# Performance work log

Hardware: AMD Instinct MI355X
Metric: run time of the kernel (lower is better)

Reference implementation:

```python
import jax, jax.numpy as jnp
import numpy as np
import math

D_MODEL = 1024
N_HEAD = 16
D_FF = 4096
B, T, S = 2, 2048, 2048
LN_EPS = 1e-5


def _linear(x, w, b):
    # torch nn.Linear: y = x @ W.T + b, W: [out, in]
    return jnp.einsum('bsd,od->bso', x, w) + b


def _layer_norm(x, g, b):
    mu = jnp.mean(x, axis=-1, keepdims=True)
    var = jnp.var(x, axis=-1, keepdims=True)
    return (x - mu) * jax.lax.rsqrt(var + LN_EPS) * g + b


def _mha(xq, xkv, wq, bq, wk, bk, wv, bv, wo, bo, mask):
    Bq, Tq, D = xq.shape
    Tk = xkv.shape[1]
    dk = D // N_HEAD
    q = _linear(xq, wq, bq).reshape(Bq, Tq, N_HEAD, dk).transpose(0, 2, 1, 3)
    k = _linear(xkv, wk, bk).reshape(Bq, Tk, N_HEAD, dk).transpose(0, 2, 1, 3)
    v = _linear(xkv, wv, bv).reshape(Bq, Tk, N_HEAD, dk).transpose(0, 2, 1, 3)
    scores = jnp.einsum('bhqd,bhkd->bhqk', q, k) / math.sqrt(dk)
    if mask is not None:
        scores = jnp.where(mask == 0, jnp.asarray(-1e9, scores.dtype), scores)
    attn = jax.nn.softmax(scores, axis=-1)  # dropout is eval-mode identity
    out = jnp.einsum('bhqk,bhkd->bhqd', attn, v)
    out = out.transpose(0, 2, 1, 3).reshape(Bq, Tq, D)
    return _linear(out, wo, bo)


def setup_inputs() -> dict:
    key = jax.random.key(0)
    ks = jax.random.split(key, 20)
    sd = 0.02

    def w(k, shape):
        return (jax.random.normal(k, shape, dtype=jnp.float32) * sd)

    inp = {
        'x': jax.random.normal(ks[0], (B, T, D_MODEL), dtype=jnp.float32),
        'enc_output': jax.random.normal(ks[1], (B, S, D_MODEL), dtype=jnp.float32),
        # causal (future) mask for self-attention
        'tgt_mask': jnp.tril(jnp.ones((T, T), dtype=jnp.int32))[None, None, :, :].repeat(B, axis=0),
        # no source padding -> all ones
        'src_tgt_mask': jnp.ones((B, 1, T, S), dtype=jnp.int32),
        'sa_wq': w(ks[2], (D_MODEL, D_MODEL)), 'sa_bq': jnp.zeros((D_MODEL,), jnp.float32),
        'sa_wk': w(ks[3], (D_MODEL, D_MODEL)), 'sa_bk': jnp.zeros((D_MODEL,), jnp.float32),
        'sa_wv': w(ks[4], (D_MODEL, D_MODEL)), 'sa_bv': jnp.zeros((D_MODEL,), jnp.float32),
        'sa_wo': w(ks[5], (D_MODEL, D_MODEL)), 'sa_bo': jnp.zeros((D_MODEL,), jnp.float32),
        'ca_wq': w(ks[6], (D_MODEL, D_MODEL)), 'ca_bq': jnp.zeros((D_MODEL,), jnp.float32),
        'ca_wk': w(ks[7], (D_MODEL, D_MODEL)), 'ca_bk': jnp.zeros((D_MODEL,), jnp.float32),
        'ca_wv': w(ks[8], (D_MODEL, D_MODEL)), 'ca_bv': jnp.zeros((D_MODEL,), jnp.float32),
        'ca_wo': w(ks[9], (D_MODEL, D_MODEL)), 'ca_bo': jnp.zeros((D_MODEL,), jnp.float32),
        'ffn_w1': w(ks[10], (D_FF, D_MODEL)), 'ffn_b1': jnp.zeros((D_FF,), jnp.float32),
        'ffn_w2': w(ks[11], (D_MODEL, D_FF)), 'ffn_b2': jnp.zeros((D_MODEL,), jnp.float32),
        'ln1_g': jnp.ones((D_MODEL,), jnp.float32), 'ln1_b': jnp.zeros((D_MODEL,), jnp.float32),
        'ln2_g': jnp.ones((D_MODEL,), jnp.float32), 'ln2_b': jnp.zeros((D_MODEL,), jnp.float32),
        'ln3_g': jnp.ones((D_MODEL,), jnp.float32), 'ln3_b': jnp.zeros((D_MODEL,), jnp.float32),
    }
    return inp


def reference(x, enc_output, tgt_mask, src_tgt_mask,
              sa_wq, sa_bq, sa_wk, sa_bk, sa_wv, sa_bv, sa_wo, sa_bo,
              ca_wq, ca_bq, ca_wk, ca_bk, ca_wv, ca_bv, ca_wo, ca_bo,
              ffn_w1, ffn_b1, ffn_w2, ffn_b2,
              ln1_g, ln1_b, ln2_g, ln2_b, ln3_g, ln3_b):
    # masked self-attention + residual + LN
    a1 = _mha(x, x, sa_wq, sa_bq, sa_wk, sa_bk, sa_wv, sa_bv, sa_wo, sa_bo, tgt_mask)
    x = _layer_norm(x + a1, ln1_g, ln1_b)
    # cross-attention + residual + LN
    a2 = _mha(x, enc_output, ca_wq, ca_bq, ca_wk, ca_bk, ca_wv, ca_bv, ca_wo, ca_bo, src_tgt_mask)
    x = _layer_norm(x + a2, ln2_g, ln2_b)
    # FFN + residual + LN
    h = jax.nn.relu(_linear(x, ffn_w1, ffn_b1))
    f = _linear(h, ffn_w2, ffn_b2)
    x = _layer_norm(x + f, ln3_g, ln3_b)
    return x
```

## Files before the change

### kernel.cpp

```cpp
#include <hip/hip_runtime.h>
#include <stdint.h>

typedef uint16_t u16;
typedef __attribute__((ext_vector_type(8))) short short8;
typedef __attribute__((ext_vector_type(4))) short short4v;
typedef __attribute__((ext_vector_type(4))) float f32x4;
typedef __attribute__((ext_vector_type(2))) unsigned int u32x2;

#define GLB_AS __attribute__((address_space(1)))
#define LDS_AS __attribute__((address_space(3)))

__device__ __forceinline__ void gload_lds16(const void* g, void* l) {
  __builtin_amdgcn_global_load_lds((GLB_AS void*)(g), (LDS_AS void*)(l), 16, 0, 0);
}

__device__ __forceinline__ float bf2f(u16 u) {
  union { uint32_t i; float f; } v; v.i = ((uint32_t)u) << 16; return v.f;
}
__device__ __forceinline__ u16 f2bf(float f) {
  uint32_t x = __builtin_bit_cast(uint32_t, f);
  return (u16)((x + 0x7fffu + ((x >> 16) & 1u)) >> 16);
}
__device__ __forceinline__ uint32_t cvtpk(float lo, float hi) {
  uint32_t r;
  asm("v_cvt_pk_bf16_f32 %0, %1, %2" : "=v"(r) : "v"(lo), "v"(hi));
  return r;
}

struct CastJobs {
  const float* s[12];
  u16* d[12];
  int n[12];
};
__global__ __launch_bounds__(256) void cast_many(CastJobs j)
{
  const int job = blockIdx.y;
  const int i = (blockIdx.x * 256 + threadIdx.x) * 4;
  if (i >= j.n[job]) return;
  const float4 v = *(const float4*)(j.s[job] + i);
  short4v r;
  r[0] = (short)f2bf(v.x); r[1] = (short)f2bf(v.y);
  r[2] = (short)f2bf(v.z); r[3] = (short)f2bf(v.w);
  *(short4v*)(j.d[job] + i) = r;
}

__global__ __launch_bounds__(256) void vtrans(
    const u16* __restrict__ V, int vs, u16* __restrict__ Vt)
{
  __shared__ u16 tl[64][72];
  const int tid = threadIdx.x;
  const int b = blockIdx.z, h = blockIdx.y, t0 = blockIdx.x * 64;
#pragma unroll
  for (int it = 0; it < 2; ++it) {
    const int r = (tid >> 3) + it*32, c = (tid & 7) * 8;
    short8 vv = *(const short8*)(V + (size_t)(b*2048 + t0 + r)*vs + h*64 + c);
    *(short8*)(&tl[r][c]) = vv;
  }
  __syncthreads();
#pragma unroll
  for (int it = 0; it < 2; ++it) {
    const int d = (tid >> 3) + it*32, t8 = (tid & 7) * 8;
    short8 ov;
#pragma unroll
    for (int j = 0; j < 8; ++j) ov[j] = (short)tl[t8 + j][d];
    *(short8*)(Vt + ((size_t)((b*16 + h)*64 + d))*2048 + t0 + t8) = ov;
  }
}

template<int RELU, int NSEG, int BN, int SCALEQ>
__global__ __launch_bounds__(256) void gemm_bt(
    const u16* __restrict__ A, const u16* __restrict__ W,
    const float* __restrict__ b0, const float* __restrict__ b1,
    const float* __restrict__ b2, u16* __restrict__ Y,
    int M, int N, int K)
{
  constexpr int NBUF = (BN == 64) ? 3 : 2;
  __shared__ __attribute__((aligned(16))) u16 lA[NBUF][128*64];
  __shared__ __attribute__((aligned(16))) u16 lB[NBUF][BN*64];
  const int tid  = threadIdx.x;
  const int lane = tid & 63, wv = tid >> 6;
  constexpr int WM = (BN == 128) ? 64 : 32;
  constexpr int MI = WM / 16;
  constexpr int BRND = BN / 32;
  const int wm = (BN == 128) ? (wv >> 1) : wv;
  const int wn = (BN == 128) ? (wv & 1) : 0;
  const int l16 = lane & 15, l4 = lane >> 4;
  const int rswz = (l16 & 7) << 4;

  const int gx = gridDim.x;
  int flat = blockIdx.y * gx + blockIdx.x;
  flat = (flat & 7) * ((gx * gridDim.y) >> 3) + (flat >> 3);
  const int bx = (flat % gx) * BN, by = (flat / gx) * 128;

  const f32x4 fzero = {0.f, 0.f, 0.f, 0.f};
  f32x4 acc[MI][4];
#pragma unroll
  for (int i = 0; i < MI; ++i)
#pragma unroll
    for (int j = 0; j < 4; ++j) acc[i][j] = fzero;

  const int o = wv*1024 + lane*16;

  auto stage = [&](int k0, int buf) {
#pragma unroll
    for (int r = 0; r < 4; ++r) {
      const int oo = r*4096 + o;
      const int row = oo >> 7;
      const int src = ((oo & 127) ^ ((row & 7) << 4)) >> 1;
      gload_lds16(A + (size_t)(by + row)*K + (k0 + src), (char*)lA[buf] + oo);
    }
#pragma unroll
    for (int r = 0; r < BRND; ++r) {
      const int oo = r*4096 + o;
      const int row = oo >> 7;
      const int src = ((oo & 127) ^ ((row & 7) << 4)) >> 1;
      gload_lds16(W + (size_t)(bx + row)*K + (k0 + src), (char*)lB[buf] + oo);
    }
  };

  auto compute = [&](int cur) {
    short8 af[2][MI], bfv[2][4];
#pragma unroll
    for (int ks = 0; ks < 2; ++ks) {
      const int cb = (ks*64 + l4*16) ^ rswz;
#pragma unroll
      for (int i = 0; i < MI; ++i)
        af[ks][i]  = *(const short8*)((const char*)lA[cur] + (wm*WM + i*16 + l16)*128 + cb);
#pragma unroll
      for (int j = 0; j < 4; ++j)
        bfv[ks][j] = *(const short8*)((const char*)lB[cur] + (wn*64 + j*16 + l16)*128 + cb);
    }
#pragma unroll
    for (int ks = 0; ks < 2; ++ks)
#pragma unroll
      for (int i = 0; i < MI; ++i)
#pragma unroll
        for (int j = 0; j < 4; ++j)
          acc[i][j] = __builtin_amdgcn_mfma_f32_16x16x32_bf16(af[ks][i], bfv[ks][j], acc[i][j], 0, 0, 0);
  };

  const int KT = K >> 6;
  if constexpr (BN == 64) {
    stage(0, 0);
    int cur = 0;
    for (int kt = 0; kt < KT; ++kt) {
      const int nxt = (cur + 1 == 3) ? 0 : cur + 1;
      if (kt + 1 < KT) {
        stage((kt + 1) << 6, nxt);
        asm volatile("s_waitcnt vmcnt(6)" ::: "memory");
      } else {
        asm volatile("s_waitcnt vmcnt(0)" ::: "memory");
      }
      __builtin_amdgcn_s_barrier();
      __builtin_amdgcn_sched_barrier(0);
      compute(cur);
      cur = nxt;
    }
  } else {
    stage(0, 0);
    for (int kt = 0; kt < KT; ++kt) {
      const int cur = kt & 1;
      __syncthreads();
      short8 af[2][MI], bfv[2][4];
#pragma unroll
      for (int ks = 0; ks < 2; ++ks) {
        const int cb = (ks*64 + l4*16) ^ rswz;
#pragma unroll
        for (int i = 0; i < MI; ++i)
          af[ks][i]  = *(const short8*)((const char*)lA[cur] + (wm*WM + i*16 + l16)*128 + cb);
#pragma unroll
        for (int j = 0; j < 4; ++j)
          bfv[ks][j] = *(const short8*)((const char*)lB[cur] + (wn*64 + j*16 + l16)*128 + cb);
      }
      if (kt + 1 < KT) stage((kt + 1) << 6, cur ^ 1);
#pragma unroll
      for (int ks = 0; ks < 2; ++ks)
#pragma unroll
        for (int i = 0; i < MI; ++i)
#pragma unroll
          for (int j = 0; j < 4; ++j)
            acc[i][j] = __builtin_amdgcn_mfma_f32_16x16x32_bf16(af[ks][i], bfv[ks][j], acc[i][j], 0, 0, 0);
    }
  }

  const float SCLF = 0.18033688f;
#pragma unroll
  for (int j = 0; j < 4; ++j) {
    const int col = bx + wn*64 + j*16 + l16;
    float bv;
    int seg = 0;
    if (NSEG == 1) bv = b0[col];
    else {
      seg = col >> 10;
      const int off = col & 1023;
      const float* bp = (seg == 0) ? b0 : ((seg == 1) ? b1 : b2);
      bv = bp[off];
    }
#pragma unroll
    for (int i = 0; i < MI; ++i) {
      const int r0 = by + wm*WM + i*16 + l4*4;
#pragma unroll
      for (int r = 0; r < 4; ++r) {
        float v = acc[i][j][r] + bv;
        if (RELU) v = v > 0.f ? v : 0.f;
        if (SCALEQ && (NSEG == 1 || seg == 0)) v *= SCLF;
        Y[(size_t)(r0 + r)*N + col] = f2bf(v);
      }
    }
  }
}

template<int CAUSAL, int QR>
__global__ __launch_bounds__(512, (QR == 16) ? 4 : 2) void attn_fwd(
    const u16* __restrict__ Q, int qs,
    const u16* __restrict__ K, int ks_,
    const u16* __restrict__ Vt, u16* __restrict__ O, int Tk)
{
  constexpr int NG = QR / 16;
  __shared__ __attribute__((aligned(16))) u16 lK[2][128*64];
  __shared__ __attribute__((aligned(16))) u16 lV[2][64*128];
  __shared__ __attribute__((aligned(16))) u16 lP[8][NG*1024];
  const int tid  = threadIdx.x;
  const int lane = tid & 63, wv = tid >> 6;
  const int l16 = lane & 15, l4 = lane >> 4;
  const int b = blockIdx.z, h = blockIdx.y;
  int strip;
  if (CAUSAL) {
    const int u = (blockIdx.x + blockIdx.z) & 15;
    strip = (u & 1) ? (15 - (u >> 1)) : (u >> 1);
  } else {
    strip = blockIdx.x;
  }
  const int Bq = strip * (8 * QR);
  const int qrow = Bq + wv*QR;

  short8 qf[NG][2];
#pragma unroll
  for (int g = 0; g < NG; ++g) {
    const u16* Qb = Q + (size_t)(b*2048 + qrow + g*16 + l16)*qs + h*64;
#pragma unroll
    for (int ks = 0; ks < 2; ++ks)
      qf[g][ks] = *(const short8*)(Qb + ks*32 + l4*8);
  }

  const f32x4 fzero = {0.f, 0.f, 0.f, 0.f};
  f32x4 accO[NG][4];
#pragma unroll
  for (int g = 0; g < NG; ++g)
#pragma unroll
    for (int i = 0; i < 4; ++i) accO[g][i] = fzero;
  float lrow[NG];
#pragma unroll
  for (int g = 0; g < NG; ++g) lrow[g] = 0.f;

  const int kend = CAUSAL ? (Bq + 8*QR) : Tk;
  const int nt = kend >> 7;
  const int qmax = qrow + QR - 1;
  const int srK = tid >> 3;
  const int scK = 8 * ((tid & 7) ^ (srK & 7));
  const int srV = tid >> 4;
  const int scV = 8 * ((tid & 15) ^ (srV & 7));
  const u16* KbG = K  + (size_t)(b*2048)*ks_ + h*64 + scK;
  const u16* VbG = Vt + ((size_t)((b*16 + h)*64 + srV))*2048 + scV;
  const int wvoff = (tid >> 6) * 1024;
  const int rswz = (l16 & 7) << 4;
  const int sbq = (lane & 48) + l4*4;

  char* const pbuf = (char*)lP + (tid >> 6) * (NG*2048);
  const int swzP = (l16 & 7) << 4;
  int wrA[4], rdA[2];
#pragma unroll
  for (int nf = 0; nf < 4; ++nf) wrA[nf] = l16*128 + ((nf*32 + l4*8) ^ swzP);
#pragma unroll
  for (int c = 0; c < 2; ++c)    rdA[c] = l16*128 + ((c*64 + l4*16) ^ swzP);

  auto readK = [&](int h2, int bb, short8 (&kf)[4][2]) {
#pragma unroll
    for (int nf = 0; nf < 4; ++nf) {
      const char* base = (const char*)lK[bb] + (h2*64 + nf*16 + l16)*128;
      kf[nf][0] = *(const short8*)(base + ((l4*16)      ^ rswz));
      kf[nf][1] = *(const short8*)(base + ((64 + l4*16) ^ rswz));
    }
  };

  auto compute64 = [&](int h2, int kvb, short8 (&kf)[4][2], int bb) {
#pragma unroll
    for (int g = 0; g < NG; ++g) {
      f32x4 sf[4];
      __builtin_amdgcn_s_setprio(1);
#pragma unroll
      for (int nf = 0; nf < 4; ++nf) {
        f32x4 s = fzero;
        s = __builtin_amdgcn_mfma_f32_16x16x32_bf16(kf[nf][0], qf[g][0], s, 0, 0, 0);
        s = __builtin_amdgcn_mfma_f32_16x16x32_bf16(kf[nf][1], qf[g][1], s, 0, 0, 0);
        sf[nf] = s;
      }
      __builtin_amdgcn_s_setprio(0);
      if (CAUSAL && (kvb + 63 > qrow + g*16)) {
        const int q = qrow + g*16 + l16;
#pragma unroll
        for (int nf = 0; nf < 4; ++nf)
#pragma unroll
          for (int r = 0; r < 4; ++r) {
            const int kv = kvb + nf*16 + l4*4 + r;
            if (kv > q) sf[nf][r] = -1e30f;
          }
      }
#pragma unroll
      for (int nf = 0; nf < 4; ++nf)
#pragma unroll
        for (int r = 0; r < 4; ++r)
          sf[nf][r] = exp2f(sf[nf][r]);
      float sm[4];
#pragma unroll
      for (int nf = 0; nf < 4; ++nf)
        sm[nf] = (sf[nf][0] + sf[nf][1]) + (sf[nf][2] + sf[nf][3]);
      lrow[g] += (sm[0] + sm[1]) + (sm[2] + sm[3]);
#pragma unroll
      for (int nf = 0; nf < 4; ++nf) {
        u32x2 w;
        w[0] = cvtpk(sf[nf][0], sf[nf][1]);
        w[1] = cvtpk(sf[nf][2], sf[nf][3]);
        *(u32x2*)(pbuf + g*2048 + wrA[nf]) = w;
      }
    }
#pragma unroll
    for (int c = 0; c < 2; ++c) {
      short8 pa[NG];
#pragma unroll
      for (int g = 0; g < NG; ++g)
        pa[g] = *(const short8*)(pbuf + g*2048 + rdA[c]);
      __builtin_amdgcn_s_setprio(1);
#pragma unroll
      for (int df = 0; df < 4; ++df) {
        const short8 vf = *(const short8*)((const char*)lV[bb] +
            (df*16 + l16)*256 + ((h2*128 + c*64 + l4*16) ^ rswz));
#pragma unroll
        for (int g = 0; g < NG; ++g)
          accO[g][df] = __builtin_amdgcn_mfma_f32_16x16x32_bf16(pa[g], vf, accO[g][df], 0, 0, 0);
      }
      __builtin_amdgcn_s_setprio(0);
    }
  };

#pragma unroll
  for (int r = 0; r < 2; ++r) {
    gload_lds16(KbG + (size_t)(r*64 + srK)*ks_, (char*)lK[0] + r*8192 + wvoff);
    gload_lds16(VbG + (size_t)(r*32)*2048,      (char*)lV[0] + r*8192 + wvoff);
  }

  for (int t = 0; t < nt; ++t) {
    const int bb = t & 1;
    const int kb = t << 7;
    __syncthreads();
    short8 kf[4][2];
    readK(0, bb, kf);
    if (t + 1 < nt) {
      const int kb2 = kb + 128;
#pragma unroll
      for (int r = 0; r < 2; ++r) {
        gload_lds16(KbG + (size_t)(kb2 + r*64 + srK)*ks_,
                    (char*)lK[bb^1] + r*8192 + wvoff);
        gload_lds16(VbG + (size_t)(r*32)*2048 + kb2,
                    (char*)lV[bb^1] + r*8192 + wvoff);
      }
    }
    compute64(0, kb, kf, bb);
    if (!CAUSAL || (kb + 64 <= qmax)) {
      readK(1, bb, kf);
      compute64(1, kb + 64, kf, bb);
    }
  }

#pragma unroll
  for (int g = 0; g < NG; ++g) {
    lrow[g] += __shfl_xor(lrow[g], 16);
    lrow[g] += __shfl_xor(lrow[g], 32);
    u16* Ob = O + (size_t)(b*2048 + qrow + g*16 + l4*4)*1024 + h*64;
#pragma unroll
    for (int r = 0; r < 4; ++r) {
      const float inv = 1.f / __shfl(lrow[g], sbq + r);
#pragma unroll
      for (int df = 0; df < 4; ++df)
        Ob[(size_t)r*1024 + df*16 + l16] = f2bf(accO[g][df][r] * inv);
    }
  }
}

template<int XF32, int OF32>
__global__ __launch_bounds__(256) void add_ln(
    const void* __restrict__ Xp, const u16* __restrict__ R,
    const float* __restrict__ G, const float* __restrict__ Bb,
    void* __restrict__ OUTp)
{
  const int row = blockIdx.x;
  const int tid = threadIdx.x;
  const size_t base = (size_t)row*1024 + tid*4;
  float xv[4];
  if (XF32) {
    const float4 t = *(const float4*)((const float*)Xp + base);
    xv[0] = t.x; xv[1] = t.y; xv[2] = t.z; xv[3] = t.w;
  } else {
    short4v t = *(const short4v*)((const u16*)Xp + base);
#pragma unroll
    for (int i = 0; i < 4; ++i) xv[i] = bf2f((u16)t[i]);
  }
  short4v rv = *(const short4v*)(R + base);
  float v[4], s = 0.f, s2 = 0.f;
#pragma unroll
  for (int i = 0; i < 4; ++i) {
    float t = xv[i] + bf2f((u16)rv[i]);
    v[i] = t; s += t; s2 += t*t;
  }
#pragma unroll
  for (int m = 1; m < 64; m <<= 1) { s += __shfl_xor(s, m); s2 += __shfl_xor(s2, m); }
  __shared__ float red[8];
  const int w = tid >> 6, lane = tid & 63;
  if (lane == 0) { red[w] = s; red[4 + w] = s2; }
  __syncthreads();
  s  = red[0] + red[1] + red[2] + red[3];
  s2 = red[4] + red[5] + red[6] + red[7];
  const float mu  = s * (1.f/1024.f);
  const float var = s2 * (1.f/1024.f) - mu*mu;
  const float rs  = rsqrtf(var + 1e-5f);
  if (OF32) {
    float4 ov;
    ov.x = (v[0]-mu)*rs*G[tid*4+0] + Bb[tid*4+0];
    ov.y = (v[1]-mu)*rs*G[tid*4+1] + Bb[tid*4+1];
    ov.z = (v[2]-mu)*rs*G[tid*4+2] + Bb[tid*4+2];
    ov.w = (v[3]-mu)*rs*G[tid*4+3] + Bb[tid*4+3];
    *(float4*)((float*)OUTp + base) = ov;
  } else {
    short4v ov;
#pragma unroll
    for (int i = 0; i < 4; ++i)
      ov[i] = (short)f2bf((v[i] - mu)*rs*G[tid*4+i] + Bb[tid*4+i]);
    *(short4v*)((u16*)OUTp + base) = ov;
  }
}

extern "C" void kernel_launch(void* const* d_in, const int* in_sizes, int n_in,
                              void* d_out, int out_size, void* d_ws, size_t ws_size,
                              hipStream_t stream)
{
  (void)in_sizes; (void)n_in; (void)out_size;
  const float* x    = (const float*)d_in[0];
  const float* enc  = (const float*)d_in[1];
  const float* sa_wq = (const float*)d_in[4];  const float* sa_bq = (const float*)d_in[5];
  const float* sa_wk = (const float*)d_in[6];  const float* sa_bk = (const float*)d_in[7];
  const float* sa_wv = (const float*)d_in[8];  const float* sa_bv = (const float*)d_in[9];
  const float* sa_wo = (const float*)d_in[10]; const float* sa_bo = (const float*)d_in[11];
  const float* ca_wq = (const float*)d_in[12]; const float* ca_bq = (const float*)d_in[13];
  const float* ca_wk = (const float*)d_in[14]; const float* ca_bk = (const float*)d_in[15];
  const float* ca_wv = (const float*)d_in[16]; const float* ca_bv = (const float*)d_in[17];
  const float* ca_wo = (const float*)d_in[18]; const float* ca_bo = (const float*)d_in[19];
  const float* w1 = (const float*)d_in[20];    const float* b1 = (const float*)d_in[21];
  const float* w2 = (const float*)d_in[22];    const float* b2 = (const float*)d_in[23];
  const float* ln1g = (const float*)d_in[24];  const float* ln1b = (const float*)d_in[25];
  const float* ln2g = (const float*)d_in[26];  const float* ln2b = (const float*)d_in[27];
  const float* ln3g = (const float*)d_in[28];  const float* ln3b = (const float*)d_in[29];
  float* out = (float*)d_out;

  char* ws = (char*)d_ws;
  const size_t MB = 1024*1024;
  u16* xb   = (u16*)(ws);
  u16* encb = (u16*)(ws + 8*MB);
  u16* wsab = (u16*)(ws + 16*MB);
  u16* wcab = (u16*)(ws + 24*MB);
  u16* x1   = (u16*)(ws + 32*MB);
  u16* ao   = (u16*)(ws + 40*MB);
  u16* tmp  = (u16*)(ws + 48*MB);
  u16* vt   = (u16*)(ws + 56*MB);
  u16* qkv  = (u16*)(ws + 64*MB);
  u16* kvb  = (u16*)(ws + 88*MB);
  u16* x2   = xb;
  u16* hb   = qkv;

  const bool bigws = ws_size >= (size_t)120*MB;
  u16* w1b = bigws ? (u16*)(ws + 104*MB) : encb;
  u16* w2b = bigws ? (u16*)(ws + 112*MB) : vt;

  const int NW = 1024*1024;
  const int NX = 4096*1024;
  dim3 blk(256);

  {
    CastJobs cj{};
    cj.s[0] = x;     cj.d[0] = xb;           cj.n[0] = NX;
    cj.s[1] = enc;   cj.d[1] = encb;         cj.n[1] = NX;
    cj.s[2] = sa_wq; cj.d[2] = wsab + 0*NW;  cj.n[2] = NW;
    cj.s[3] = sa_wk; cj.d[3] = wsab + 1*NW;  cj.n[3] = NW;
    cj.s[4] = sa_wv; cj.d[4] = wsab + 2*NW;  cj.n[4] = NW;
    cj.s[5] = sa_wo; cj.d[5] = wsab + 3*NW;  cj.n[5] = NW;
    cj.s[6] = ca_wq; cj.d[6] = wcab + 0*NW;  cj.n[6] = NW;
    cj.s[7] = ca_wk; cj.d[7] = wcab + 1*NW;  cj.n[7] = NW;
    cj.s[8] = ca_wv; cj.d[8] = wcab + 2*NW;  cj.n[8] = NW;
    cj.s[9] = ca_wo; cj.d[9] = wcab + 3*NW;  cj.n[9] = NW;
    int njobs = 10;
    if (bigws) {
      cj.s[10] = w1; cj.d[10] = w1b; cj.n[10] = NX;
      cj.s[11] = w2; cj.d[11] = w2b; cj.n[11] = NX;
      njobs = 12;
    }
    cast_many<<<dim3(NX/1024, njobs), blk, 0, stream>>>(cj);
  }

  const int M = 4096;
  dim3 gN64(16, 32);
  dim3 gQKV(24, 32);
  dim3 gKV(16, 32);
  dim3 gF1(32, 32);
  dim3 gAttn(16, 16, 2);
  dim3 gT(32, 16, 2);
  dim3 blk512(512);

  gemm_bt<0,3,128,1><<<gQKV, blk, 0, stream>>>(xb, wsab, sa_bq, sa_bk, sa_bv, qkv, M, 3072, 1024);
  vtrans<<<gT, blk, 0, stream>>>(qkv + 2048, 3072, vt);
  attn_fwd<1,16><<<gAttn, blk512, 0, stream>>>(qkv, 3072, qkv + 1024, 3072, vt, ao, 2048);
  gemm_bt<0,1,64,0><<<gN64, blk, 0, stream>>>(ao, wsab + 3*NW, sa_bo, sa_bo, sa_bo, tmp, M, 1024, 1024);
  add_ln<1,0><<<4096, blk, 0, stream>>>(x, tmp, ln1g, ln1b, x1);

  gemm_bt<0,1,64,1><<<gN64, blk, 0, stream>>>(x1, wcab + 0*NW, ca_bq, ca_bq, ca_bq, qkv, M, 1024, 1024);
  gemm_bt<0,2,128,0><<<gKV, blk, 0, stream>>>(encb, wcab + 1*NW, ca_bk, ca_bv, ca_bv, kvb, M, 2048, 1024);
  vtrans<<<gT, blk, 0, stream>>>(kvb + 1024, 2048, vt);
  attn_fwd<0,16><<<gAttn, blk512, 0, stream>>>(qkv, 1024, kvb, 2048, vt, ao, 2048);
  if (!bigws) {
    CastJobs cj{};
    cj.s[0] = w1; cj.d[0] = w1b; cj.n[0] = NX;
    cj.s[1] = w2; cj.d[1] = w2b; cj.n[1] = NX;
    cast_many<<<dim3(NX/1024, 2), blk, 0, stream>>>(cj);
  }
  gemm_bt<0,1,64,0><<<gN64, blk, 0, stream>>>(ao, wcab + 3*NW, ca_bo, ca_bo, ca_bo, tmp, M, 1024, 1024);
  add_ln<0,0><<<4096, blk, 0, stream>>>(x1, tmp, ln2g, ln2b, x2);

  gemm_bt<1,1,128,0><<<gF1, blk, 0, stream>>>(x2, w1b, b1, b1, b1, hb, M, 4096, 1024);
  gemm_bt<0,1,64,0><<<gN64, blk, 0, stream>>>(hb, w2b, b2, b2, b2, tmp, M, 1024, 4096);
  add_ln<0,1><<<4096, blk, 0, stream>>>(x2, tmp, ln3g, ln3b, out);
}
```

Before: 327.7 us.

## Load K/V fragments directly from global in attention, drop LDS staging

Rewrites the attention kernel to use 256-thread blocks that each cover 64 query rows. K and V^T MFMA fragments now come straight from global memory into registers, with K prefetched one 64-key tile ahead, instead of being double-buffered through LDS with async global-to-LDS loads and block barriers. This removes the __syncthreads and LDS traffic for K/V and doubles the number of blocks in the grid. In exchange each wave re-reads K/V from global/L2 independently, losing sharing across waves, and the loads are strided rows rather than coalesced tiles.

```diff
diff --git a/kernel.cpp b/kernel.cpp
--- a/kernel.cpp
+++ b/kernel.cpp
@@ -210,63 +210,54 @@
   }
 }
 
-template<int CAUSAL, int QR>
-__global__ __launch_bounds__(512, (QR == 16) ? 4 : 2) void attn_fwd(
+template<int CAUSAL>
+__global__ __launch_bounds__(256) void attn_fwd(
     const u16* __restrict__ Q, int qs,
     const u16* __restrict__ K, int ks_,
     const u16* __restrict__ Vt, u16* __restrict__ O, int Tk)
 {
-  constexpr int NG = QR / 16;
-  __shared__ __attribute__((aligned(16))) u16 lK[2][128*64];
-  __shared__ __attribute__((aligned(16))) u16 lV[2][64*128];
-  __shared__ __attribute__((aligned(16))) u16 lP[8][NG*1024];
+  __shared__ __attribute__((aligned(16))) u16 lP[4][1024];
   const int tid  = threadIdx.x;
   const int lane = tid & 63, wv = tid >> 6;
   const int l16 = lane & 15, l4 = lane >> 4;
   const int b = blockIdx.z, h = blockIdx.y;
   int strip;
   if (CAUSAL) {
-    const int u = (blockIdx.x + blockIdx.z) & 15;
-    strip = (u & 1) ? (15 - (u >> 1)) : (u >> 1);
+    const int u = (blockIdx.x + blockIdx.z) & 31;
+    strip = (u & 1) ? (31 - (u >> 1)) : (u >> 1);
   } else {
     strip = blockIdx.x;
   }
-  const int Bq = strip * (8 * QR);
-  const int qrow = Bq + wv*QR;
-
-  short8 qf[NG][2];
-#pragma unroll
-  for (int g = 0; g < NG; ++g) {
-    const u16* Qb = Q + (size_t)(b*2048 + qrow + g*16 + l16)*qs + h*64;
-#pragma unroll
-    for (int ks = 0; ks < 2; ++ks)
-      qf[g][ks] = *(const short8*)(Qb + ks*32 + l4*8);
-  }
+  const int Bq = strip * 64;
+  const int qrow = Bq + wv*16;
+
+  const u16* Qb = Q + (size_t)(b*2048 + qrow + l16)*qs + h*64;
+  short8 qf[2];
+#pragma unroll
+  for (int ks = 0; ks < 2; ++ks)
+    qf[ks] = *(const short8*)(Qb + ks*32 + l4*8);
 
   const f32x4 fzero = {0.f, 0.f, 0.f, 0.f};
-  f32x4 accO[NG][4];
-#pragma unroll
-  for (int g = 0; g < NG; ++g)
-#pragma unroll
-    for (int i = 0; i < 4; ++i) accO[g][i] = fzero;
-  float lrow[NG];
-#pragma unroll
-  for (int g = 0; g < NG; ++g) lrow[g] = 0.f;
-
-  const int kend = CAUSAL ? (Bq + 8*QR) : Tk;
-  const int nt = kend >> 7;
-  const int qmax = qrow + QR - 1;
-  const int srK = tid >> 3;
-  const int scK = 8 * ((tid & 7) ^ (srK & 7));
-  const int srV = tid >> 4;
-  const int scV = 8 * ((tid & 15) ^ (srV & 7));
-  const u16* KbG = K  + (size_t)(b*2048)*ks_ + h*64 + scK;
-  const u16* VbG = Vt + ((size_t)((b*16 + h)*64 + srV))*2048 + scV;
-  const int wvoff = (tid >> 6) * 1024;
-  const int rswz = (l16 & 7) << 4;
+  f32x4 accO[4];
+#pragma unroll
+  for (int i = 0; i < 4; ++i) accO[i] = fzero;
+  float lrow = 0.f;
+
+  const int kend = CAUSAL ? (Bq + 64) : Tk;
+  const int nt = kend >> 6;
   const int sbq = (lane & 48) + l4*4;
 
-  char* const pbuf = (char*)lP + (tid >> 6) * (NG*2048);
+  const u16* kp[4];
+#pragma unroll
+  for (int nf = 0; nf < 4; ++nf)
+    kp[nf] = K + (size_t)(b*2048 + nf*16 + l16)*ks_ + h*64 + l4*8;
+  const size_t kinc = (size_t)64 * ks_;
+  const u16* vp[4];
+#pragma unroll
+  for (int df = 0; df < 4; ++df)
+    vp[df] = Vt + ((size_t)((b*16 + h)*64 + df*16 + l16))*2048 + l4*8;
+
+  char* const pbuf = (char*)lP + wv*2048;
   const int swzP = (l16 & 7) << 4;
   int wrA[4], rdA[2];
 #pragma unroll
@@ -274,116 +265,88 @@
 #pragma unroll
   for (int c = 0; c < 2; ++c)    rdA[c] = l16*128 + ((c*64 + l4*16) ^ swzP);
 
-  auto readK = [&](int h2, int bb, short8 (&kf)[4][2]) {
+  short8 kf[4][2];
+#pragma unroll
+  for (int nf = 0; nf < 4; ++nf) {
+    kf[nf][0] = *(const short8*)(kp[nf]);
+    kf[nf][1] = *(const short8*)(kp[nf] + 32);
+    kp[nf] += kinc;
+  }
+
+  for (int t = 0; t < nt; ++t) {
+    const int kvb = t << 6;
+    f32x4 sf[4];
+    __builtin_amdgcn_s_setprio(1);
 #pragma unroll
     for (int nf = 0; nf < 4; ++nf) {
-      const char* base = (const char*)lK[bb] + (h2*64 + nf*16 + l16)*128;
-      kf[nf][0] = *(const short8*)(base + ((l4*16)      ^ rswz));
-      kf[nf][1] = *(const short8*)(base + ((64 + l4*16) ^ rswz));
-    }
-  };
-
-  auto compute64 = [&](int h2, int kvb, short8 (&kf)[4][2], int bb) {
-#pragma unroll
-    for (int g = 0; g < NG; ++g) {
-      f32x4 sf[4];
+      f32x4 s = fzero;
+      s = __builtin_amdgcn_mfma_f32_16x16x32_bf16(kf[nf][0], qf[0], s, 0, 0, 0);
+      s = __builtin_amdgcn_mfma_f32_16x16x32_bf16(kf[nf][1], qf[1], s, 0, 0, 0);
+      sf[nf] = s;
+    }
+    __builtin_amdgcn_s_setprio(0);
+    if (t + 1 < nt) {
+#pragma unroll
+      for (int nf = 0; nf < 4; ++nf) {
+        kf[nf][0] = *(const short8*)(kp[nf]);
+        kf[nf][1] = *(const short8*)(kp[nf] + 32);
+        kp[nf] += kinc;
+      }
+    }
+    short8 vf[4][2];
+#pragma unroll
+    for (int df = 0; df < 4; ++df) {
+      vf[df][0] = *(const short8*)(vp[df]);
+      vf[df][1] = *(const short8*)(vp[df] + 32);
+      vp[df] += 64;
+    }
+    if (CAUSAL && (kvb + 63 > qrow)) {
+      const int q = qrow + l16;
+#pragma unroll
+      for (int nf = 0; nf < 4; ++nf)
+#pragma unroll
+        for (int r = 0; r < 4; ++r) {
+          const int kv = kvb + nf*16 + l4*4 + r;
+          if (kv > q) sf[nf][r] = -1e30f;
+        }
+    }
+#pragma unroll
+    for (int nf = 0; nf < 4; ++nf)
+#pragma unroll
+      for (int r = 0; r < 4; ++r)
+        sf[nf][r] = exp2f(sf[nf][r]);
+    float sm[4];
+#pragma unroll
+    for (int nf = 0; nf < 4; ++nf)
+      sm[nf] = (sf[nf][0] + sf[nf][1]) + (sf[nf][2] + sf[nf][3]);
+    lrow += (sm[0] + sm[1]) + (sm[2] + sm[3]);
+#pragma unroll
+    for (int nf = 0; nf < 4; ++nf) {
+      u32x2 w;
+      w[0] = cvtpk(sf[nf][0], sf[nf][1]);
+      w[1] = cvtpk(sf[nf][2], sf[nf][3]);
+      *(u32x2*)(pbuf + wrA[nf]) = w;
+    }
+#pragma unroll
+    for (int c = 0; c < 2; ++c) {
+      const short8 pa = *(const short8*)(pbuf + rdA[c]);
       __builtin_amdgcn_s_setprio(1);
 #pragma unroll
-      for (int nf = 0; nf < 4; ++nf) {
-        f32x4 s = fzero;
-        s = __builtin_amdgcn_mfma_f32_16x16x32_bf16(kf[nf][0], qf[g][0], s, 0, 0, 0);
-        s = __builtin_amdgcn_mfma_f32_16x16x32_bf16(kf[nf][1], qf[g][1], s, 0, 0, 0);
-        sf[nf] = s;
-      }
+      for (int df = 0; df < 4; ++df)
+        accO[df] = __builtin_amdgcn_mfma_f32_16x16x32_bf16(pa, vf[df][c], accO[df], 0, 0, 0);
       __builtin_amdgcn_s_setprio(0);
-      if (CAUSAL && (kvb + 63 > qrow + g*16)) {
-        const int q = qrow + g*16 + l16;
-#pragma unroll
-        for (int nf = 0; nf < 4; ++nf)
-#pragma unroll
-          for (int r = 0; r < 4; ++r) {
-            const int kv = kvb + nf*16 + l4*4 + r;
-            if (kv > q) sf[nf][r] = -1e30f;
-          }
-      }
-#pragma unroll
-      for (int nf = 0; nf < 4; ++nf)
-#pragma unroll
-        for (int r = 0; r < 4; ++r)
-          sf[nf][r] = exp2f(sf[nf][r]);
-      float sm[4];
-#pragma unroll
-      for (int nf = 0; nf < 4; ++nf)
-        sm[nf] = (sf[nf][0] + sf[nf][1]) + (sf[nf][2] + sf[nf][3]);
-      lrow[g] += (sm[0] + sm[1]) + (sm[2] + sm[3]);
-#pragma unroll
-      for (int nf = 0; nf < 4; ++nf) {
-        u32x2 w;
-        w[0] = cvtpk(sf[nf][0], sf[nf][1]);
-        w[1] = cvtpk(sf[nf][2], sf[nf][3]);
-        *(u32x2*)(pbuf + g*2048 + wrA[nf]) = w;
-      }
-    }
-#pragma unroll
-    for (int c = 0; c < 2; ++c) {
-      short8 pa[NG];
-#pragma unroll
-      for (int g = 0; g < NG; ++g)
-        pa[g] = *(const short8*)(pbuf + g*2048 + rdA[c]);
-      __builtin_amdgcn_s_setprio(1);
-#pragma unroll
-      for (int df = 0; df < 4; ++df) {
-        const short8 vf = *(const short8*)((const char*)lV[bb] +
-            (df*16 + l16)*256 + ((h2*128 + c*64 + l4*16) ^ rswz));
-#pragma unroll
-        for (int g = 0; g < NG; ++g)
-          accO[g][df] = __builtin_amdgcn_mfma_f32_16x16x32_bf16(pa[g], vf, accO[g][df], 0, 0, 0);
-      }
-      __builtin_amdgcn_s_setprio(0);
-    }
-  };
-
-#pragma unroll
-  for (int r = 0; r < 2; ++r) {
-    gload_lds16(KbG + (size_t)(r*64 + srK)*ks_, (char*)lK[0] + r*8192 + wvoff);
-    gload_lds16(VbG + (size_t)(r*32)*2048,      (char*)lV[0] + r*8192 + wvoff);
-  }
-
-  for (int t = 0; t < nt; ++t) {
-    const int bb = t & 1;
-    const int kb = t << 7;
-    __syncthreads();
-    short8 kf[4][2];
-    readK(0, bb, kf);
-    if (t + 1 < nt) {
-      const int kb2 = kb + 128;
-#pragma unroll
-      for (int r = 0; r < 2; ++r) {
-        gload_lds16(KbG + (size_t)(kb2 + r*64 + srK)*ks_,
-                    (char*)lK[bb^1] + r*8192 + wvoff);
-        gload_lds16(VbG + (size_t)(r*32)*2048 + kb2,
-                    (char*)lV[bb^1] + r*8192 + wvoff);
-      }
-    }
-    compute64(0, kb, kf, bb);
-    if (!CAUSAL || (kb + 64 <= qmax)) {
-      readK(1, bb, kf);
-      compute64(1, kb + 64, kf, bb);
-    }
-  }
-
-#pragma unroll
-  for (int g = 0; g < NG; ++g) {
-    lrow[g] += __shfl_xor(lrow[g], 16);
-    lrow[g] += __shfl_xor(lrow[g], 32);
-    u16* Ob = O + (size_t)(b*2048 + qrow + g*16 + l4*4)*1024 + h*64;
-#pragma unroll
-    for (int r = 0; r < 4; ++r) {
-      const float inv = 1.f / __shfl(lrow[g], sbq + r);
-#pragma unroll
-      for (int df = 0; df < 4; ++df)
-        Ob[(size_t)r*1024 + df*16 + l16] = f2bf(accO[g][df][r] * inv);
-    }
+    }
+  }
+
+  lrow += __shfl_xor(lrow, 16);
+  lrow += __shfl_xor(lrow, 32);
+  u16* Ob = O + (size_t)(b*2048 + qrow + l4*4)*1024 + h*64;
+#pragma unroll
+  for (int r = 0; r < 4; ++r) {
+    const float inv = 1.f / __shfl(lrow, sbq + r);
+#pragma unroll
+    for (int df = 0; df < 4; ++df)
+      Ob[(size_t)r*1024 + df*16 + l16] = f2bf(accO[df][r] * inv);
   }
 }
 
@@ -510,20 +473,19 @@
   dim3 gQKV(24, 32);
   dim3 gKV(16, 32);
   dim3 gF1(32, 32);
-  dim3 gAttn(16, 16, 2);
+  dim3 gAttn(32, 16, 2);
   dim3 gT(32, 16, 2);
-  dim3 blk512(512);
 
   gemm_bt<0,3,128,1><<<gQKV, blk, 0, stream>>>(xb, wsab, sa_bq, sa_bk, sa_bv, qkv, M, 3072, 1024);
   vtrans<<<gT, blk, 0, stream>>>(qkv + 2048, 3072, vt);
-  attn_fwd<1,16><<<gAttn, blk512, 0, stream>>>(qkv, 3072, qkv + 1024, 3072, vt, ao, 2048);
+  attn_fwd<1><<<gAttn, blk, 0, stream>>>(qkv, 3072, qkv + 1024, 3072, vt, ao, 2048);
   gemm_bt<0,1,64,0><<<gN64, blk, 0, stream>>>(ao, wsab + 3*NW, sa_bo, sa_bo, sa_bo, tmp, M, 1024, 1024);
   add_ln<1,0><<<4096, blk, 0, stream>>>(x, tmp, ln1g, ln1b, x1);
 
   gemm_bt<0,1,64,1><<<gN64, blk, 0, stream>>>(x1, wcab + 0*NW, ca_bq, ca_bq, ca_bq, qkv, M, 1024, 1024);
   gemm_bt<0,2,128,0><<<gKV, blk, 0, stream>>>(encb, wcab + 1*NW, ca_bk, ca_bv, ca_bv, kvb, M, 2048, 1024);
   vtrans<<<gT, blk, 0, stream>>>(kvb + 1024, 2048, vt);
-  attn_fwd<0,16><<<gAttn, blk512, 0, stream>>>(qkv, 1024, kvb, 2048, vt, ao, 2048);
+  attn_fwd<0><<<gAttn, blk, 0, stream>>>(qkv, 1024, kvb, 2048, vt, ao, 2048);
   if (!bigws) {
     CastJobs cj{};
     cj.s[0] = w1; cj.d[0] = w1b; cj.n[0] = NX;
```

Result: slower. 592.9 us (+80.9%).
